# Performance work log

Measured on AMD Instinct MI355X. Metric: run time of the kernel, lower is better.

## Reference

```python
import jax, jax.numpy as jnp
import numpy as np

EPS = 1e-12  # matches torch F.normalize default eps


def _l2_normalize(x):
    norm = jnp.linalg.norm(x, axis=-1, keepdims=True)
    return x / jnp.maximum(norm, EPS)


def setup_inputs() -> dict:
    key = jax.random.key(0)
    kq, kd = jax.random.split(key)
    query_embeds = jax.random.normal(kq, (64, 768), dtype=jnp.float32)
    doc_embeds = jax.random.normal(kd, (500000, 768), dtype=jnp.float32)
    return {"query_embeds": query_embeds, "doc_embeds": doc_embeds, "top_k": 10}


def reference(query_embeds, doc_embeds, top_k):
    # compute_scores: L2-normalize both sides, cosine similarity GEMM
    q = _l2_normalize(query_embeds)            # [Q, D]
    d = _l2_normalize(doc_embeds)              # [N, D]
    scores = jnp.einsum('qd,nd->qn', q, d)     # [Q, N]
    k = min(top_k, scores.shape[1])
    top_scores, top_indices = jax.lax.top_k(scores, k)
    return top_indices, top_scores
```

## Files before the change

### kernel.cpp

```cpp
#include <hip/hip_runtime.h>
#include <math.h>

#define DD 768
#define QN 64
#define TN 128
#define BK 64
#define NSLICE (DD / BK)
#define TOPK 10
#define CAND 32
#define NBLK 512

typedef short bf16x8 __attribute__((ext_vector_type(8)));
typedef float f32x4  __attribute__((ext_vector_type(4)));

__device__ __forceinline__ unsigned short f2bf(float f) {
    unsigned int u = __float_as_uint(f);
    u = (u + 0x7fffu + ((u >> 16) & 1u)) >> 16;
    return (unsigned short)u;
}

__device__ __forceinline__ void topk_insert(float (&sc)[TOPK], int (&id)[TOPK],
                                            float v, int nid) {
    if (v <= sc[TOPK - 1]) return;
#pragma unroll
    for (int j = TOPK - 1; j >= 1; --j) {
        bool gtj   = v > sc[j];
        bool gtjm1 = v > sc[j - 1];
        float cs = gtjm1 ? sc[j - 1] : v;
        int   ci = gtjm1 ? id[j - 1] : nid;
        sc[j] = gtj ? cs : sc[j];
        id[j] = gtj ? ci : id[j];
    }
    bool gt0 = v > sc[0];
    sc[0] = gt0 ? v : sc[0];
    id[0] = gt0 ? nid : id[0];
}

__global__ void qnorm_kernel(const float* __restrict__ q,
                             unsigned short* __restrict__ qn) {
    const int row = blockIdx.x;
    const int t = threadIdx.x;
    float vals[3];
    float s = 0.f;
#pragma unroll
    for (int i = 0; i < 3; ++i) {
        vals[i] = q[row * DD + i * 256 + t];
        s += vals[i] * vals[i];
    }
#pragma unroll
    for (int o = 32; o; o >>= 1) s += __shfl_down(s, o);
    __shared__ float red[4];
    if ((t & 63) == 0) red[t >> 6] = s;
    __syncthreads();
    float tot = red[0] + red[1] + red[2] + red[3];
    float inv = 1.f / fmaxf(sqrtf(tot), 1e-12f);
#pragma unroll
    for (int i = 0; i < 3; ++i)
        qn[row * DD + i * 256 + t] = f2bf(vals[i] * inv);
}

__global__ __launch_bounds__(256, 2)
void score_kernel(const unsigned short* __restrict__ qn,
                  const float* __restrict__ docs,
                  float* __restrict__ cand_sc, int* __restrict__ cand_id,
                  int Ndocs, int ntiles) {
    __shared__ unsigned short atile[QN * BK];
    __shared__ unsigned short btile[TN * BK];
    __shared__ float scb[QN * 133];
    __shared__ float dnormp[TN * 8];
    __shared__ float dinv[TN];

    const int tid  = threadIdx.x;
    const int lane = tid & 63;
    const int wv   = tid >> 6;
    const int r0   = tid >> 3;
    const int c8   = tid & 7;

    float sc[TOPK];
    int   id[TOPK];
#pragma unroll
    for (int j = 0; j < TOPK; ++j) { sc[j] = -INFINITY; id[j] = 0; }

    for (int tile = blockIdx.x; tile < ntiles; tile += gridDim.x) {
        const int d0g = tile * TN;

        f32x4 acc[4][2];
#pragma unroll
        for (int m = 0; m < 4; ++m)
#pragma unroll
            for (int n = 0; n < 2; ++n)
#pragma unroll
                for (int v = 0; v < 4; ++v) acc[m][n][v] = 0.f;
        float dnp[4] = {0.f, 0.f, 0.f, 0.f};

        float4 rb[4][2];
        uint4  ra[2];

        auto LOADB = [&](int kk) {
#pragma unroll
            for (int i = 0; i < 4; ++i) {
                int row = i * 32 + r0;
                int gd = d0g + row;
                if (gd < Ndocs) {
                    const float* p = docs + (size_t)gd * DD + kk + c8 * 8;
                    rb[i][0] = *(const float4*)(p);
                    rb[i][1] = *(const float4*)(p + 4);
                } else {
                    rb[i][0] = make_float4(0.f, 0.f, 0.f, 0.f);
                    rb[i][1] = make_float4(0.f, 0.f, 0.f, 0.f);
                }
            }
        };
        auto LOADA = [&](int kk) {
#pragma unroll
            for (int i = 0; i < 2; ++i) {
                int row = i * 32 + r0;
                ra[i] = *(const uint4*)(qn + row * DD + kk + c8 * 8);
            }
        };
        auto STORE = [&]() {
#pragma unroll
            for (int i = 0; i < 2; ++i) {
                int row = i * 32 + r0;
                int off = (row * 128 + c8 * 16) ^ ((row & 7) << 4);
                *(uint4*)((char*)atile + off) = ra[i];
            }
#pragma unroll
            for (int i = 0; i < 4; ++i) {
                int row = i * 32 + r0;
                float4 a = rb[i][0], b = rb[i][1];
                dnp[i] += a.x * a.x + a.y * a.y + a.z * a.z + a.w * a.w
                        + b.x * b.x + b.y * b.y + b.z * b.z + b.w * b.w;
                uint4 w;
                w.x = (unsigned)f2bf(a.x) | ((unsigned)f2bf(a.y) << 16);
                w.y = (unsigned)f2bf(a.z) | ((unsigned)f2bf(a.w) << 16);
                w.z = (unsigned)f2bf(b.x) | ((unsigned)f2bf(b.y) << 16);
                w.w = (unsigned)f2bf(b.z) | ((unsigned)f2bf(b.w) << 16);
                int off = (row * 128 + c8 * 16) ^ ((row & 7) << 4);
                *(uint4*)((char*)btile + off) = w;
            }
        };

        LOADA(0);
        LOADB(0);
        for (int s = 0; s < NSLICE; ++s) {
            __syncthreads();
            STORE();
            if (s + 1 < NSLICE) {
                LOADA((s + 1) * BK);
                LOADB((s + 1) * BK);
            }
            __syncthreads();
            const int fr = lane & 15, fk = lane >> 4;
#pragma unroll
            for (int kc = 0; kc < 2; ++kc) {
                bf16x8 af[4];
#pragma unroll
                for (int m = 0; m < 4; ++m) {
                    int row = m * 16 + fr;
                    int off = (row * 128 + kc * 64 + fk * 16) ^ ((row & 7) << 4);
                    af[m] = *(const bf16x8*)((const char*)atile + off);
                }
                bf16x8 bfr[2];
#pragma unroll
                for (int n = 0; n < 2; ++n) {
                    int row = wv * 32 + n * 16 + fr;
                    int off = (row * 128 + kc * 64 + fk * 16) ^ ((row & 7) << 4);
                    bfr[n] = *(const bf16x8*)((const char*)btile + off);
                }
#pragma unroll
                for (int m = 0; m < 4; ++m)
#pragma unroll
                    for (int n = 0; n < 2; ++n)
                        acc[m][n] = __builtin_amdgcn_mfma_f32_16x16x32_bf16(
                            af[m], bfr[n], acc[m][n], 0, 0, 0);
            }
        }

        __syncthreads();
#pragma unroll
        for (int i = 0; i < 4; ++i)
            dnormp[(i * 32 + r0) * 8 + c8] = dnp[i];
        __syncthreads();
        if (tid < TN) {
            float s = 0.f;
#pragma unroll
            for (int j = 0; j < 8; ++j) s += dnormp[tid * 8 + j];
            dinv[tid] = 1.f / fmaxf(sqrtf(s), 1e-12f);
        }
        __syncthreads();

        {
            const int fr = lane & 15, fq4 = (lane >> 4) * 4;
#pragma unroll
            for (int m = 0; m < 4; ++m)
#pragma unroll
                for (int n = 0; n < 2; ++n) {
                    int dcol = wv * 32 + n * 16 + fr;
                    float di = dinv[dcol];
#pragma unroll
                    for (int v = 0; v < 4; ++v)
                        scb[(m * 16 + fq4 + v) * 133 + dcol] = acc[m][n][v] * di;
                }
        }
        __syncthreads();

        if (tid < QN) {
            int rem = Ndocs - d0g;
            if (rem > TN) rem = TN;
            for (int j = 0; j < rem; ++j)
                topk_insert(sc, id, scb[tid * 133 + j], d0g + j);
        }
    }

    if (tid < QN) {
        size_t base = ((size_t)blockIdx.x * QN + tid) * TOPK;
#pragma unroll
        for (int j = 0; j < TOPK; ++j) {
            cand_sc[base + j] = sc[j];
            cand_id[base + j] = id[j];
        }
    }
}

__global__ __launch_bounds__(256)
void merge32_kernel(const float* __restrict__ cand_sc,
                    const int* __restrict__ cand_id,
                    int* __restrict__ cand32, int nlists) {
    const int q = blockIdx.x;
    const int t = threadIdx.x;
    __shared__ float lsc[256 * CAND];
    __shared__ int   lid[256 * CAND];

    {
        const bool hasA = t < nlists, hasB = t + 256 < nlists;
        const size_t baseA = ((size_t)t * QN + q) * TOPK;
        const size_t baseB = ((size_t)(t + 256) * QN + q) * TOPK;
        int ia = 0, ib = 0;
        float va = hasA ? cand_sc[baseA] : -INFINITY;
        int   xa = hasA ? cand_id[baseA] : 0;
        float vb = hasB ? cand_sc[baseB] : -INFINITY;
        int   xb = hasB ? cand_id[baseB] : 0;
        for (int j = 0; j < 2 * TOPK; ++j) {
            bool ta = va >= vb;
            lsc[t * CAND + j] = ta ? va : vb;
            lid[t * CAND + j] = ta ? xa : xb;
            if (ta) {
                ++ia;
                bool ok = hasA && ia < TOPK;
                va = ok ? cand_sc[baseA + ia] : -INFINITY;
                xa = ok ? cand_id[baseA + ia] : 0;
            } else {
                ++ib;
                bool ok = hasB && ib < TOPK;
                vb = ok ? cand_sc[baseB + ib] : -INFINITY;
                xb = ok ? cand_id[baseB + ib] : 0;
            }
        }
        for (int j = 2 * TOPK; j < CAND; ++j) {
            lsc[t * CAND + j] = -INFINITY;
            lid[t * CAND + j] = 0;
        }
    }
    __syncthreads();

    for (int s = 128; s >= 1; s >>= 1) {
        if (t < s) {
            int ia = 0, ib = 0;
            float rs[CAND];
            int   ri[CAND];
#pragma unroll
            for (int j = 0; j < CAND; ++j) {
                float va = lsc[t * CAND + ia];
                float vb = lsc[(t + s) * CAND + ib];
                bool ta = va >= vb;
                rs[j] = ta ? va : vb;
                ri[j] = ta ? lid[t * CAND + ia] : lid[(t + s) * CAND + ib];
                ia += ta ? 1 : 0;
                ib += ta ? 0 : 1;
            }
#pragma unroll
            for (int j = 0; j < CAND; ++j) {
                lsc[t * CAND + j] = rs[j];
                lid[t * CAND + j] = ri[j];
            }
        }
        __syncthreads();
    }
    if (t < CAND) cand32[q * CAND + t] = lid[t];
}

__global__ __launch_bounds__(256)
void rescore_kernel(const float* __restrict__ q, const float* __restrict__ docs,
                    const int* __restrict__ cand32, float* __restrict__ out,
                    int score_off) {
    const int qi = blockIdx.x;
    const int t = threadIdx.x, lane = t & 63, wv = t >> 6;
    __shared__ float qbuf[DD];
    __shared__ float red[4];
    __shared__ float csc[CAND];
    __shared__ int   cid[CAND];

    float v[3];
    float ss = 0.f;
#pragma unroll
    for (int i = 0; i < 3; ++i) {
        v[i] = q[qi * DD + i * 256 + t];
        ss += v[i] * v[i];
    }
#pragma unroll
    for (int o = 32; o; o >>= 1) ss += __shfl_down(ss, o);
    if (lane == 0) red[wv] = ss;
    __syncthreads();
    float qnorm = fmaxf(sqrtf(red[0] + red[1] + red[2] + red[3]), 1e-12f);
#pragma unroll
    for (int i = 0; i < 3; ++i) qbuf[i * 256 + t] = v[i] / qnorm;
    __syncthreads();

    for (int c = wv; c < CAND; c += 4) {
        const int d = cand32[qi * CAND + c];
        const float* dp = docs + (size_t)d * DD;
        float dss = 0.f;
#pragma unroll
        for (int j = 0; j < 3; ++j) {
            float4 dv = *(const float4*)(dp + j * 256 + lane * 4);
            dss += dv.x * dv.x + dv.y * dv.y + dv.z * dv.z + dv.w * dv.w;
        }
#pragma unroll
        for (int o = 32; o; o >>= 1) dss += __shfl_down(dss, o);
        dss = __shfl(dss, 0);
        float dnorm = fmaxf(sqrtf(dss), 1e-12f);
        double dot = 0.0;
#pragma unroll
        for (int j = 0; j < 3; ++j) {
            float4 dv = *(const float4*)(dp + j * 256 + lane * 4);
            float4 qv = *(const float4*)(qbuf + j * 256 + lane * 4);
            float d0 = dv.x / dnorm, d1 = dv.y / dnorm;
            float d2 = dv.z / dnorm, d3 = dv.w / dnorm;
            dot += (double)d0 * qv.x + (double)d1 * qv.y
                 + (double)d2 * qv.z + (double)d3 * qv.w;
        }
#pragma unroll
        for (int o = 32; o; o >>= 1) dot += __shfl_down(dot, o);
        if (lane == 0) { csc[c] = (float)dot; cid[c] = d; }
    }
    __syncthreads();

    if (t < CAND) {
        float s = csc[t];
        int myid = cid[t];
        int rank = 0;
        for (int j = 0; j < CAND; ++j) {
            float sj = csc[j];
            int ij = cid[j];
            rank += ((sj > s) || (sj == s && ij < myid)) ? 1 : 0;
        }
        if (rank < TOPK) {
            out[qi * TOPK + rank] = (float)myid;
            out[score_off + qi * TOPK + rank] = s;
        }
    }
}

extern "C" void kernel_launch(void* const* d_in, const int* in_sizes, int n_in,
                              void* d_out, int out_size, void* d_ws, size_t ws_size,
                              hipStream_t stream) {
    const float* q    = (const float*)d_in[0];
    const float* docs = (const float*)d_in[1];
    const int N = in_sizes[1] / DD;

    unsigned short* qn = (unsigned short*)d_ws;
    const size_t qbytes = (size_t)QN * DD * 2;
    int* cand32 = (int*)((char*)d_ws + qbytes);
    const size_t c32bytes = (size_t)QN * CAND * 4;

    size_t used = qbytes + c32bytes;
    size_t avail = (ws_size > used) ? (ws_size - used) : 0;
    size_t per_list = (size_t)QN * TOPK * 8;
    int ntiles = (N + TN - 1) / TN;
    int nblk = NBLK;
    if ((size_t)nblk * per_list > avail) nblk = (int)(avail / per_list);
    if (nblk < 1) nblk = 1;
    if (nblk > ntiles) nblk = ntiles;

    float* cand_sc = (float*)((char*)d_ws + used);
    int*   cand_id = (int*)(cand_sc + (size_t)nblk * QN * TOPK);

    hipLaunchKernelGGL(qnorm_kernel, dim3(QN), dim3(256), 0, stream, q, qn);
    hipLaunchKernelGGL(score_kernel, dim3(nblk), dim3(256), 0, stream,
                       qn, docs, cand_sc, cand_id, N, ntiles);
    hipLaunchKernelGGL(merge32_kernel, dim3(QN), dim3(256), 0, stream,
                       cand_sc, cand_id, cand32, nblk);
    hipLaunchKernelGGL(rescore_kernel, dim3(QN), dim3(256), 0, stream,
                       q, docs, cand32, (float*)d_out, out_size / 2);
}
```

Baseline: 471.4 us.

## Double-buffer doc tiles, read query fragments from global, parallelize per-tile top-k

Restructures the score kernel so the doc tile uses two LDS buffers with a register prefetch, leaving one barrier per K-slice instead of two. The next tile's first slices are loaded while the current tile's top-k runs. Query fragments are now read straight from global/L2 rather than staged in LDS. The LDS arena is shared between buffers and scores to allow 3 blocks per CU, and the grid grows to 768 blocks. Top-k selection is spread across all 256 threads (4 per query) with a block-level reduction, and the merge kernel switches to insertion into a 32-entry list. The costs are more global traffic for query reads and higher register pressure under the tighter launch bounds.

```diff
diff --git a/kernel.cpp b/kernel.cpp
--- a/kernel.cpp
+++ b/kernel.cpp
@@ -1,14 +1,15 @@
 #include <hip/hip_runtime.h>
+#include <hip/hip_bf16.h>
 #include <math.h>
 
 #define DD 768
 #define QN 64
 #define TN 128
 #define BK 64
-#define NSLICE (DD / BK)
+#define NSLICE 12
 #define TOPK 10
 #define CAND 32
-#define NBLK 512
+#define NBLK 768
 
 typedef short bf16x8 __attribute__((ext_vector_type(8)));
 typedef float f32x4  __attribute__((ext_vector_type(4)));
@@ -17,6 +18,13 @@
     unsigned int u = __float_as_uint(f);
     u = (u + 0x7fffu + ((u >> 16) & 1u)) >> 16;
     return (unsigned short)u;
+}
+
+__device__ __forceinline__ unsigned pk2(float a, float b) {
+    union { __hip_bfloat162 h2; unsigned u; } cv;
+    cv.h2.x = __float2bfloat16(a);
+    cv.h2.y = __float2bfloat16(b);
+    return cv.u;
 }
 
 __device__ __forceinline__ void topk_insert(float (&sc)[TOPK], int (&id)[TOPK],
@@ -59,30 +67,74 @@
         qn[row * DD + i * 256 + t] = f2bf(vals[i] * inv);
 }
 
-__global__ __launch_bounds__(256, 2)
+__global__ __launch_bounds__(256, 3)
 void score_kernel(const unsigned short* __restrict__ qn,
                   const float* __restrict__ docs,
                   float* __restrict__ cand_sc, int* __restrict__ cand_id,
                   int Ndocs, int ntiles) {
-    __shared__ unsigned short atile[QN * BK];
-    __shared__ unsigned short btile[TN * BK];
-    __shared__ float scb[QN * 133];
-    __shared__ float dnormp[TN * 8];
+    __shared__ float arena_f[8832];
     __shared__ float dinv[TN];
+    char* arena = (char*)arena_f;
+    unsigned short* bt0 = (unsigned short*)arena;
+    unsigned short* bt1 = (unsigned short*)(arena + 16384);
+    float* scb = arena_f;
 
     const int tid  = threadIdx.x;
     const int lane = tid & 63;
     const int wv   = tid >> 6;
     const int r0   = tid >> 3;
     const int c8   = tid & 7;
+    const int fr   = lane & 15;
+    const int fk   = lane >> 4;
+    const int sq   = wv * 16 + (lane >> 2);
+    const int scq  = lane & 3;
+    const int sqsw = sq ^ ((scq & 1) << 4);
 
     float sc[TOPK];
     int   id[TOPK];
 #pragma unroll
     for (int j = 0; j < TOPK; ++j) { sc[j] = -INFINITY; id[j] = 0; }
 
-    for (int tile = blockIdx.x; tile < ntiles; tile += gridDim.x) {
+    float4 rb0[4][2], rb1[4][2];
+
+    auto LOADB = [&](float4 (&r)[4][2], int dg, int kk, bool full) {
+        if (full) {
+#pragma unroll
+            for (int i = 0; i < 4; ++i) {
+                const float* p = docs + (size_t)(dg + i * 32 + r0) * DD + kk + c8 * 8;
+                r[i][0] = *(const float4*)(p);
+                r[i][1] = *(const float4*)(p + 4);
+            }
+        } else {
+#pragma unroll
+            for (int i = 0; i < 4; ++i) {
+                int gd = dg + i * 32 + r0;
+                if (gd < Ndocs) {
+                    const float* p = docs + (size_t)gd * DD + kk + c8 * 8;
+                    r[i][0] = *(const float4*)(p);
+                    r[i][1] = *(const float4*)(p + 4);
+                } else {
+                    r[i][0] = make_float4(0.f, 0.f, 0.f, 0.f);
+                    r[i][1] = make_float4(0.f, 0.f, 0.f, 0.f);
+                }
+            }
+        }
+    };
+
+    int tile = blockIdx.x;
+    if (tile < ntiles) {
+        bool f0 = tile * TN + TN <= Ndocs;
+        LOADB(rb0, tile * TN, 0, f0);
+        LOADB(rb1, tile * TN, BK, f0);
+    }
+
+    for (; tile < ntiles; tile += gridDim.x) {
         const int d0g = tile * TN;
+        const bool full = d0g + TN <= Ndocs;
+        const int ntile = tile + gridDim.x;
+        const bool has_next = ntile < ntiles;
+        const int nd0 = ntile * TN;
+        const bool nfull = nd0 + TN <= Ndocs;
 
         f32x4 acc[4][2];
 #pragma unroll
@@ -93,80 +145,36 @@
                 for (int v = 0; v < 4; ++v) acc[m][n][v] = 0.f;
         float dnp[4] = {0.f, 0.f, 0.f, 0.f};
 
-        float4 rb[4][2];
-        uint4  ra[2];
-
-        auto LOADB = [&](int kk) {
+        auto STORE = [&](float4 (&r)[4][2], unsigned short* buf) {
 #pragma unroll
             for (int i = 0; i < 4; ++i) {
                 int row = i * 32 + r0;
-                int gd = d0g + row;
-                if (gd < Ndocs) {
-                    const float* p = docs + (size_t)gd * DD + kk + c8 * 8;
-                    rb[i][0] = *(const float4*)(p);
-                    rb[i][1] = *(const float4*)(p + 4);
-                } else {
-                    rb[i][0] = make_float4(0.f, 0.f, 0.f, 0.f);
-                    rb[i][1] = make_float4(0.f, 0.f, 0.f, 0.f);
-                }
-            }
-        };
-        auto LOADA = [&](int kk) {
-#pragma unroll
-            for (int i = 0; i < 2; ++i) {
-                int row = i * 32 + r0;
-                ra[i] = *(const uint4*)(qn + row * DD + kk + c8 * 8);
-            }
-        };
-        auto STORE = [&]() {
-#pragma unroll
-            for (int i = 0; i < 2; ++i) {
-                int row = i * 32 + r0;
-                int off = (row * 128 + c8 * 16) ^ ((row & 7) << 4);
-                *(uint4*)((char*)atile + off) = ra[i];
-            }
-#pragma unroll
-            for (int i = 0; i < 4; ++i) {
-                int row = i * 32 + r0;
-                float4 a = rb[i][0], b = rb[i][1];
+                float4 a = r[i][0], b = r[i][1];
                 dnp[i] += a.x * a.x + a.y * a.y + a.z * a.z + a.w * a.w
                         + b.x * b.x + b.y * b.y + b.z * b.z + b.w * b.w;
                 uint4 w;
-                w.x = (unsigned)f2bf(a.x) | ((unsigned)f2bf(a.y) << 16);
-                w.y = (unsigned)f2bf(a.z) | ((unsigned)f2bf(a.w) << 16);
-                w.z = (unsigned)f2bf(b.x) | ((unsigned)f2bf(b.y) << 16);
-                w.w = (unsigned)f2bf(b.z) | ((unsigned)f2bf(b.w) << 16);
+                w.x = pk2(a.x, a.y);
+                w.y = pk2(a.z, a.w);
+                w.z = pk2(b.x, b.y);
+                w.w = pk2(b.z, b.w);
                 int off = (row * 128 + c8 * 16) ^ ((row & 7) << 4);
-                *(uint4*)((char*)btile + off) = w;
+                *(uint4*)((char*)buf + off) = w;
             }
         };
 
-        LOADA(0);
-        LOADB(0);
-        for (int s = 0; s < NSLICE; ++s) {
-            __syncthreads();
-            STORE();
-            if (s + 1 < NSLICE) {
-                LOADA((s + 1) * BK);
-                LOADB((s + 1) * BK);
-            }
-            __syncthreads();
-            const int fr = lane & 15, fk = lane >> 4;
+        auto MM = [&](const unsigned short* buf, int kk) {
 #pragma unroll
             for (int kc = 0; kc < 2; ++kc) {
                 bf16x8 af[4];
 #pragma unroll
-                for (int m = 0; m < 4; ++m) {
-                    int row = m * 16 + fr;
-                    int off = (row * 128 + kc * 64 + fk * 16) ^ ((row & 7) << 4);
-                    af[m] = *(const bf16x8*)((const char*)atile + off);
-                }
+                for (int m = 0; m < 4; ++m)
+                    af[m] = *(const bf16x8*)(qn + (m * 16 + fr) * DD + kk + kc * 32 + fk * 8);
                 bf16x8 bfr[2];
 #pragma unroll
                 for (int n = 0; n < 2; ++n) {
                     int row = wv * 32 + n * 16 + fr;
                     int off = (row * 128 + kc * 64 + fk * 16) ^ ((row & 7) << 4);
-                    bfr[n] = *(const bf16x8*)((const char*)btile + off);
+                    bfr[n] = *(const bf16x8*)((const char*)buf + off);
                 }
 #pragma unroll
                 for (int m = 0; m < 4; ++m)
@@ -175,50 +183,93 @@
                         acc[m][n] = __builtin_amdgcn_mfma_f32_16x16x32_bf16(
                             af[m], bfr[n], acc[m][n], 0, 0, 0);
             }
-        }
-
+        };
+
+        for (int s = 0; s < NSLICE; s += 2) {
+            STORE(rb0, bt0);
+            __syncthreads();
+            if (s + 2 < NSLICE) LOADB(rb0, d0g, (s + 2) * BK, full);
+            MM(bt0, s * BK);
+
+            STORE(rb1, bt1);
+            __syncthreads();
+            if (s + 3 < NSLICE) LOADB(rb1, d0g, (s + 3) * BK, full);
+            MM(bt1, s * BK + BK);
+        }
+
+#pragma unroll
+        for (int i = 0; i < 4; ++i) {
+            float s = dnp[i];
+            s += __shfl_xor(s, 1);
+            s += __shfl_xor(s, 2);
+            s += __shfl_xor(s, 4);
+            if (c8 == 0) dinv[i * 32 + r0] = 1.f / fmaxf(sqrtf(s), 1e-12f);
+        }
         __syncthreads();
-#pragma unroll
-        for (int i = 0; i < 4; ++i)
-            dnormp[(i * 32 + r0) * 8 + c8] = dnp[i];
+
+        {
+            const int fq4 = (lane >> 4) * 4;
+#pragma unroll
+            for (int n = 0; n < 2; ++n) {
+                int dcol = wv * 32 + n * 16 + fr;
+                float di = dinv[dcol];
+                int swz = ((dcol >> 5) & 1) << 4;
+#pragma unroll
+                for (int m = 0; m < 4; ++m) {
+                    f32x4 v = acc[m][n];
+                    float4 o = make_float4(v[0] * di, v[1] * di, v[2] * di, v[3] * di);
+                    *(float4*)(scb + dcol * 68 + ((m * 16 + fq4) ^ swz)) = o;
+                }
+            }
+        }
         __syncthreads();
-        if (tid < TN) {
-            float s = 0.f;
-#pragma unroll
-            for (int j = 0; j < 8; ++j) s += dnormp[tid * 8 + j];
-            dinv[tid] = 1.f / fmaxf(sqrtf(s), 1e-12f);
-        }
-        __syncthreads();
+
+        if (has_next) {
+            LOADB(rb0, nd0, 0, nfull);
+            LOADB(rb1, nd0, BK, nfull);
+        }
 
         {
-            const int fr = lane & 15, fq4 = (lane >> 4) * 4;
-#pragma unroll
-            for (int m = 0; m < 4; ++m)
-#pragma unroll
-                for (int n = 0; n < 2; ++n) {
-                    int dcol = wv * 32 + n * 16 + fr;
-                    float di = dinv[dcol];
-#pragma unroll
-                    for (int v = 0; v < 4; ++v)
-                        scb[(m * 16 + fq4 + v) * 133 + dcol] = acc[m][n][v] * di;
-                }
-        }
-        __syncthreads();
-
-        if (tid < QN) {
             int rem = Ndocs - d0g;
             if (rem > TN) rem = TN;
-            for (int j = 0; j < rem; ++j)
-                topk_insert(sc, id, scb[tid * 133 + j], d0g + j);
-        }
-    }
-
-    if (tid < QN) {
-        size_t base = ((size_t)blockIdx.x * QN + tid) * TOPK;
+            int lim = rem - scq * 32;
+            lim = lim < 0 ? 0 : (lim > 32 ? 32 : lim);
+            for (int i = 0; i < lim; ++i) {
+                int j = scq * 32 + i;
+                topk_insert(sc, id, scb[j * 68 + sqsw], d0g + j);
+            }
+        }
+        __syncthreads();
+    }
+
+    {
+        float* lsc = arena_f;
+        int*   lid = (int*)(arena + 10240);
 #pragma unroll
         for (int j = 0; j < TOPK; ++j) {
-            cand_sc[base + j] = sc[j];
-            cand_id[base + j] = id[j];
+            lsc[tid * TOPK + j] = sc[j];
+            lid[tid * TOPK + j] = id[j];
+        }
+        __syncthreads();
+        if (tid < QN) {
+            float fs[TOPK];
+            int   fi[TOPK];
+#pragma unroll
+            for (int j = 0; j < TOPK; ++j) { fs[j] = -INFINITY; fi[j] = 0; }
+            for (int c = 0; c < 4; ++c) {
+                int base = (tid * 4 + c) * TOPK;
+                for (int j = 0; j < TOPK; ++j) {
+                    float v = lsc[base + j];
+                    if (v <= fs[TOPK - 1]) break;
+                    topk_insert(fs, fi, v, lid[base + j]);
+                }
+            }
+            size_t gbase = ((size_t)blockIdx.x * QN + tid) * TOPK;
+#pragma unroll
+            for (int j = 0; j < TOPK; ++j) {
+                cand_sc[gbase + j] = fs[j];
+                cand_id[gbase + j] = fi[j];
+            }
         }
     }
 }
@@ -231,35 +282,24 @@
     const int t = threadIdx.x;
     __shared__ float lsc[256 * CAND];
     __shared__ int   lid[256 * CAND];
-
-    {
-        const bool hasA = t < nlists, hasB = t + 256 < nlists;
-        const size_t baseA = ((size_t)t * QN + q) * TOPK;
-        const size_t baseB = ((size_t)(t + 256) * QN + q) * TOPK;
-        int ia = 0, ib = 0;
-        float va = hasA ? cand_sc[baseA] : -INFINITY;
-        int   xa = hasA ? cand_id[baseA] : 0;
-        float vb = hasB ? cand_sc[baseB] : -INFINITY;
-        int   xb = hasB ? cand_id[baseB] : 0;
-        for (int j = 0; j < 2 * TOPK; ++j) {
-            bool ta = va >= vb;
-            lsc[t * CAND + j] = ta ? va : vb;
-            lid[t * CAND + j] = ta ? xa : xb;
-            if (ta) {
-                ++ia;
-                bool ok = hasA && ia < TOPK;
-                va = ok ? cand_sc[baseA + ia] : -INFINITY;
-                xa = ok ? cand_id[baseA + ia] : 0;
-            } else {
-                ++ib;
-                bool ok = hasB && ib < TOPK;
-                vb = ok ? cand_sc[baseB + ib] : -INFINITY;
-                xb = ok ? cand_id[baseB + ib] : 0;
-            }
-        }
-        for (int j = 2 * TOPK; j < CAND; ++j) {
-            lsc[t * CAND + j] = -INFINITY;
-            lid[t * CAND + j] = 0;
+    const int base = t * CAND;
+#pragma unroll
+    for (int j = 0; j < CAND; ++j) { lsc[base + j] = -INFINITY; lid[base + j] = 0; }
+
+    for (int b = t; b < nlists; b += 256) {
+        size_t g = ((size_t)b * QN + q) * TOPK;
+        for (int j = 0; j < TOPK; ++j) {
+            float v = cand_sc[g + j];
+            if (v <= lsc[base + CAND - 1]) break;
+            int idv = cand_id[g + j];
+            int p = CAND - 1;
+            while (p > 0 && lsc[base + p - 1] < v) {
+                lsc[base + p] = lsc[base + p - 1];
+                lid[base + p] = lid[base + p - 1];
+                --p;
+            }
+            lsc[base + p] = v;
+            lid[base + p] = idv;
         }
     }
     __syncthreads();
```

Result: slower. 1.158 ms (+145.6%).
